# Performance work log

Hardware: AMD Instinct MI355X
Metric: run time of the kernel (lower is better)

Reference implementation:

```python
import jax, jax.numpy as jnp
import numpy as np

D = 256      # channels / model dim
HEADS = 8
DK = 32
DV = 32
B, H, W = 8, 32, 32
EPS = 1e-5


def setup_inputs() -> dict:
    key = jax.random.key(0)
    ks = jax.random.split(key, 9)
    s = 0.02
    return {
        "x":  jax.random.normal(ks[0], (B, D, H, W), dtype=jnp.float32),
        "Wq": jax.random.normal(ks[1], (HEADS * DK, D), dtype=jnp.float32) * s,
        "bq": jnp.zeros((HEADS * DK,), dtype=jnp.float32),
        "Wk": jax.random.normal(ks[2], (HEADS * DK, D), dtype=jnp.float32) * s,
        "bk": jnp.zeros((HEADS * DK,), dtype=jnp.float32),
        "Wv": jax.random.normal(ks[3], (HEADS * DV, D), dtype=jnp.float32) * s,
        "bv": jnp.zeros((HEADS * DV,), dtype=jnp.float32),
        "Wo": jax.random.normal(ks[4], (D, HEADS * DK), dtype=jnp.float32) * s,
        "bo": jnp.zeros((D,), dtype=jnp.float32),
    }


def reference(x, Wq, bq, Wk, bk, Wv, bv, Wo, bo):
    b, c, h, w = x.shape
    n = h * w
    # LayerNorm over [c, h, w] per sample, no affine (functional.layer_norm default)
    mu = jnp.mean(x, axis=(1, 2, 3), keepdims=True)
    var = jnp.var(x, axis=(1, 2, 3), keepdims=True)
    xn = (x - mu) * jax.lax.rsqrt(var + EPS)
    xr = xn.reshape(b, c, n).transpose(0, 2, 1)  # [b, n, c]

    def proj(Wt, bt, dh):
        y = xr @ Wt.T + bt                        # [b, n, heads*dh]
        return y.reshape(b, n, HEADS, dh).transpose(0, 2, 1, 3)  # [b, heads, n, dh]

    q = proj(Wq, bq, DK)
    k = proj(Wk, bk, DK)
    v = proj(Wv, bv, DV)

    scores = jnp.einsum('bhid,bhjd->bhij', q, k) * (DK ** -0.5)  # [b, heads, n, n]
    att = jax.nn.softmax(scores, axis=-1)
    tmp = jnp.einsum('bhij,bhjd->bhid', att, v)                  # [b, heads, n, dv]
    tmp = tmp.transpose(0, 2, 1, 3).reshape(b, n, HEADS * DV)    # [b, n, heads*dv]
    out = tmp @ Wo.T + bo                                        # [b, n, d]
    # NOTE: original does a raw .view(b, d, h, w) WITHOUT permuting — faithful reshape
    out = out.reshape(b, c, h, w)
    return out + x
```

## Files before the change

kernel.cpp:

```cpp
#include <hip/hip_runtime.h>
#include <stdint.h>

typedef unsigned short u16;
typedef unsigned int u32;
typedef __attribute__((ext_vector_type(8))) short bf16x8;
typedef __attribute__((ext_vector_type(4))) float f32x4;
typedef __attribute__((ext_vector_type(16))) float f32x16;

#define NTOK 1024
#define DMODEL 256
#define NHEAD 8
#define DK 32
#define NBATCH 8
#define PER_B (DMODEL * NTOK)

__device__ __forceinline__ float b2f(u16 h) {
    union { unsigned u; float f; } c; c.u = ((unsigned)h) << 16; return c.f;
}
__device__ __forceinline__ u16 f2b(float f) {
    unsigned u = __float_as_uint(f);
    unsigned r = u + 0x7fffu + ((u >> 16) & 1u);
    return (u16)(r >> 16);
}

__global__ void prep(const float* __restrict__ Wq, const float* __restrict__ Wk,
                     const float* __restrict__ Wv, const float* __restrict__ Wo,
                     u16* __restrict__ wb,
                     const float* __restrict__ x, float* __restrict__ part) {
    int bx = blockIdx.x;
    int t = threadIdx.x;
    if (bx < 256) {
        int m = bx >> 6;
        const float* W = (m == 0) ? Wq : (m == 1) ? Wk : (m == 2) ? Wv : Wo;
        int i = ((bx & 63) * 256 + t) * 4;
        float4 v = *(const float4*)&W[i];
        ushort4 o;
        o.x = f2b(v.x); o.y = f2b(v.y); o.z = f2b(v.z); o.w = f2b(v.w);
        *(ushort4*)&wb[m * 65536 + i] = o;
        return;
    }
    int blk = bx - 256;
    int b = blk >> 3, sl = blk & 7;
    int w = t >> 6, l = t & 63;
    const float* xb = x + (size_t)b * PER_B + sl * (PER_B / 8);
    float s = 0.f, ss = 0.f;
    for (int base = 0; base < PER_B / 8; base += 1024) {
        float4 v = *(const float4*)&xb[base + t * 4];
        s += v.x + v.y + v.z + v.w;
        ss += v.x * v.x + v.y * v.y + v.z * v.z + v.w * v.w;
    }
    for (int d = 1; d < 64; d <<= 1) {
        s += __shfl_xor(s, d, 64);
        ss += __shfl_xor(ss, d, 64);
    }
    __shared__ float red[2][4];
    if (l == 0) { red[0][w] = s; red[1][w] = ss; }
    __syncthreads();
    if (t == 0) {
        float S = red[0][0] + red[0][1] + red[0][2] + red[0][3];
        float SS = red[1][0] + red[1][1] + red[1][2] + red[1][3];
        part[(b * 8 + sl) * 2] = S;
        part[(b * 8 + sl) * 2 + 1] = SS;
    }
}

__global__ void normT(const float* __restrict__ x, const float* __restrict__ part,
                      u16* __restrict__ xn) {
    int b = blockIdx.z;
    int n0 = blockIdx.x * 32;
    int c0 = blockIdx.y * 32;
    int tx = threadIdx.x, ty = threadIdx.y;
    __shared__ float s_mu, s_rs;
    __shared__ float tile[32][33];
    if (tx == 0 && ty == 0) {
        float S = 0.f, SS = 0.f;
        for (int i = 0; i < 8; ++i) { S += part[(b * 8 + i) * 2]; SS += part[(b * 8 + i) * 2 + 1]; }
        float mu = S / (float)PER_B;
        float var = SS / (float)PER_B - mu * mu;
        s_mu = mu;
        s_rs = rsqrtf(var + 1e-5f);
    }
    __syncthreads();
    float mu = s_mu, rs = s_rs;
    const float* xb = x + (size_t)b * PER_B;
#pragma unroll
    for (int i = 0; i < 4; ++i) {
        int c = c0 + ty + i * 8;
        tile[ty + i * 8][tx] = (xb[c * NTOK + n0 + tx] - mu) * rs;
    }
    __syncthreads();
    u16* xnb = xn + (size_t)b * PER_B;
#pragma unroll
    for (int i = 0; i < 4; ++i) {
        int n = n0 + ty + i * 8;
        xnb[n * DMODEL + c0 + tx] = f2b(tile[tx][ty + i * 8]);
    }
}

__global__ __launch_bounds__(256, 4) void qkv_gemm(
    const u16* __restrict__ xn, const u16* __restrict__ wb,
    const float* __restrict__ bq, const float* __restrict__ bk,
    const float* __restrict__ bv,
    u16* __restrict__ qo, u16* __restrict__ ko, u16* __restrict__ vo) {
    int mt = blockIdx.x;
    int ot = blockIdx.y;
    int b = blockIdx.z;
    int sel = ot >> 2;
    int o0 = (ot & 3) * 64;
    const u16* W = wb + sel * 65536;
    const float* bias = (sel == 0) ? bq : (sel == 1) ? bk : bv;

    __shared__ u16 As[2][64][40];
    __shared__ u16 Bs[2][64][40];
    int t = threadIdx.x;
    int w = t >> 6, l = t & 63;
    int lr = t >> 2;
    int lc = (t & 3) * 8;
    int qd = l >> 4, ln = l & 15;

    const u16* xb = xn + ((size_t)b * NTOK + mt * 64) * DMODEL;

    {
        uint4 a0 = *(const uint4*)&xb[lr * DMODEL + lc];
        uint4 b0 = *(const uint4*)&W[(o0 + lr) * DMODEL + lc];
        *(uint4*)&As[0][lr][lc] = a0;
        *(uint4*)&Bs[0][lr][lc] = b0;
    }
    __syncthreads();

    f32x4 acc[4] = {};
#pragma unroll
    for (int kb = 0; kb < 8; ++kb) {
        int cur = kb & 1;
        uint4 a1, b1;
        if (kb < 7) {
            a1 = *(const uint4*)&xb[lr * DMODEL + (kb + 1) * 32 + lc];
            b1 = *(const uint4*)&W[(o0 + lr) * DMODEL + (kb + 1) * 32 + lc];
        }
        bf16x8 af = *(const bf16x8*)&As[cur][w * 16 + ln][qd * 8];
#pragma unroll
        for (int ns = 0; ns < 4; ++ns) {
            bf16x8 bf = *(const bf16x8*)&Bs[cur][ns * 16 + ln][qd * 8];
            acc[ns] = __builtin_amdgcn_mfma_f32_16x16x32_bf16(af, bf, acc[ns], 0, 0, 0);
        }
        if (kb < 7) {
            *(uint4*)&As[cur ^ 1][lr][lc] = a1;
            *(uint4*)&Bs[cur ^ 1][lr][lc] = b1;
            __syncthreads();
        }
    }
    if (sel == 0) {
        const float scale = 0.25505654344884634f;
#pragma unroll
        for (int ns = 0; ns < 4; ++ns) {
            int o = o0 + ns * 16 + ln;
            float bias_f = bias[o];
            int head = o >> 5, d = o & 31;
#pragma unroll
            for (int r = 0; r < 4; ++r) {
                int n_row = mt * 64 + w * 16 + qd * 4 + r;
                float v = (acc[ns][r] + bias_f) * scale;
                qo[(((size_t)b * NHEAD + head) * NTOK + n_row) * DK + d] = f2b(v);
            }
        }
    } else if (sel == 1) {
#pragma unroll
        for (int ns = 0; ns < 4; ++ns) {
            int o = o0 + ns * 16 + ln;
            float bias_f = bias[o];
            int head = o >> 5, d = o & 31;
            int dh = d >> 4, h8 = (d >> 3) & 1, j = d & 7;
            size_t base = (size_t)(b * NHEAD + head) * 32768;
#pragma unroll
            for (int r = 0; r < 4; ++r) {
                int n_row = mt * 64 + w * 16 + qd * 4 + r;
                int c = n_row >> 5, w5 = n_row & 31;
                int kslot = (w5 & 19) | ((w5 & 4) << 1) | ((w5 & 8) >> 1);
                float v = acc[ns][r] + bias_f;
                ko[base + ((size_t)((c * 2 + dh) * 2 + h8)) * 256 + kslot * 8 + j] = f2b(v);
            }
        }
    } else {
        int n0 = mt * 64 + w * 16 + qd * 4;
        int c = n0 >> 5, w5 = n0 & 31;
        int grp = (w5 >> 4) & 1, h8 = (w5 >> 3) & 1, j = w5 & 7;
#pragma unroll
        for (int ns = 0; ns < 4; ++ns) {
            int o = o0 + ns * 16 + ln;
            float bias_f = bias[o];
            int head = o >> 5, d = o & 31;
            ushort4 pk;
            pk.x = f2b(acc[ns][0] + bias_f);
            pk.y = f2b(acc[ns][1] + bias_f);
            pk.z = f2b(acc[ns][2] + bias_f);
            pk.w = f2b(acc[ns][3] + bias_f);
            size_t base = (size_t)(b * NHEAD + head) * 32768;
            *(ushort4*)&vo[base + ((size_t)((c * 2 + grp) * 2 + h8)) * 256 + d * 8 + j] = pk;
        }
    }
}

__global__ __launch_bounds__(256, 4) void attn(
    const u16* __restrict__ qws, const u16* __restrict__ kpan,
    const u16* __restrict__ vpan, u16* __restrict__ tmp) {
    int bh = blockIdx.x;
    int qp = blockIdx.y;
    int b = bh >> 3, h = bh & 7;
    const u16* Q  = qws + (size_t)bh * NTOK * DK;
    const u16* Kp = kpan + (size_t)bh * 32768;
    const u16* Vp = vpan + (size_t)bh * 32768;

    __shared__ float xl[2][64];
    __shared__ float xo[2][64][17];

    int t = threadIdx.x;
    int w = t >> 6, l = t & 63;
    int qsub = w >> 1, khalf = w & 1;
    int l31 = l & 31, hi = l >> 5;

    int q0 = qp * 64 + qsub * 32;
    int c0 = khalf * 16;

    bf16x8 qf0 = *(const bf16x8*)&Q[(q0 + l31) * DK + hi * 8];
    bf16x8 qf1 = *(const bf16x8*)&Q[(q0 + l31) * DK + 16 + hi * 8];

    const u16* kb = Kp + (size_t)c0 * 1024 + hi * 256 + l31 * 8;
    const u16* vb = Vp + (size_t)c0 * 1024 + hi * 256 + l31 * 8;

    f32x16 oacc = {};
    float lsum = 0.f;

#pragma unroll
    for (int c = 0; c < 16; ++c) {
        bf16x8 kf0 = *(const bf16x8*)&kb[c * 1024];
        bf16x8 kf1 = *(const bf16x8*)&kb[c * 1024 + 512];
        bf16x8 va  = *(const bf16x8*)&vb[c * 1024];
        bf16x8 vg  = *(const bf16x8*)&vb[c * 1024 + 512];

        f32x16 s = {};
        s = __builtin_amdgcn_mfma_f32_32x32x16_bf16(kf0, qf0, s, 0, 0, 0);
        s = __builtin_amdgcn_mfma_f32_32x32x16_bf16(kf1, qf1, s, 0, 0, 0);

        union { u32 u[4]; bf16x8 v; } pa, pb;
        float ps = 0.f;
#pragma unroll
        for (int j = 0; j < 4; ++j) {
            float e0 = __builtin_amdgcn_exp2f(s[2 * j]);
            float e1 = __builtin_amdgcn_exp2f(s[2 * j + 1]);
            float e2 = __builtin_amdgcn_exp2f(s[2 * j + 8]);
            float e3 = __builtin_amdgcn_exp2f(s[2 * j + 9]);
            ps += (e0 + e1) + (e2 + e3);
            pa.u[j] = __builtin_amdgcn_perm(__float_as_uint(e1), __float_as_uint(e0), 0x07060302u);
            pb.u[j] = __builtin_amdgcn_perm(__float_as_uint(e3), __float_as_uint(e2), 0x07060302u);
        }
        lsum += ps;

        oacc = __builtin_amdgcn_mfma_f32_32x32x16_bf16(va, pa.v, oacc, 0, 0, 0);
        oacc = __builtin_amdgcn_mfma_f32_32x32x16_bf16(vg, pb.v, oacc, 0, 0, 0);
    }

    if (khalf == 1) {
        xl[qsub][l] = lsum;
#pragma unroll
        for (int r = 0; r < 16; ++r) xo[qsub][l][r] = oacc[r];
    }
    __syncthreads();
    if (khalf == 0) {
        lsum += xl[qsub][l];
#pragma unroll
        for (int r = 0; r < 16; ++r) oacc[r] += xo[qsub][l][r];
        lsum += __shfl_xor(lsum, 32, 64);
        float linv = 1.0f / lsum;
        int qg = q0 + l31;
        u16* op = tmp + ((size_t)b * NTOK + qg) * DMODEL + h * DK;
#pragma unroll
        for (int g = 0; g < 4; ++g) {
            ushort4 pk;
            pk.x = f2b(oacc[g * 4 + 0] * linv);
            pk.y = f2b(oacc[g * 4 + 1] * linv);
            pk.z = f2b(oacc[g * 4 + 2] * linv);
            pk.w = f2b(oacc[g * 4 + 3] * linv);
            *(ushort4*)&op[g * 8 + hi * 4] = pk;
        }
    }
}

__global__ __launch_bounds__(256, 4) void oproj(
    const u16* __restrict__ tmp, const u16* __restrict__ wb,
    const float* __restrict__ bo, const float* __restrict__ x,
    float* __restrict__ out) {
    int mt = blockIdx.x;
    int ot = blockIdx.y;
    int b = blockIdx.z;
    const u16* Wo = wb + 3 * 65536;

    __shared__ u16 As[2][64][40];
    __shared__ u16 Bs[2][64][40];
    int t = threadIdx.x;
    int w = t >> 6, l = t & 63;
    int lr = t >> 2;
    int lc = (t & 3) * 8;
    int qd = l >> 4, ln = l & 15;

    const u16* ab = tmp + ((size_t)b * NTOK + mt * 64) * DMODEL;

    {
        uint4 a0 = *(const uint4*)&ab[lr * DMODEL + lc];
        uint4 b0 = *(const uint4*)&Wo[(ot * 64 + lr) * DMODEL + lc];
        *(uint4*)&As[0][lr][lc] = a0;
        *(uint4*)&Bs[0][lr][lc] = b0;
    }
    __syncthreads();

    f32x4 acc[4] = {};
#pragma unroll
    for (int kb = 0; kb < 8; ++kb) {
        int cur = kb & 1;
        uint4 a1, b1;
        if (kb < 7) {
            a1 = *(const uint4*)&ab[lr * DMODEL + (kb + 1) * 32 + lc];
            b1 = *(const uint4*)&Wo[(ot * 64 + lr) * DMODEL + (kb + 1) * 32 + lc];
        }
        bf16x8 af = *(const bf16x8*)&As[cur][w * 16 + ln][qd * 8];
#pragma unroll
        for (int ns = 0; ns < 4; ++ns) {
            bf16x8 bf = *(const bf16x8*)&Bs[cur][ns * 16 + ln][qd * 8];
            acc[ns] = __builtin_amdgcn_mfma_f32_16x16x32_bf16(af, bf, acc[ns], 0, 0, 0);
        }
        if (kb < 7) {
            *(uint4*)&As[cur ^ 1][lr][lc] = a1;
            *(uint4*)&Bs[cur ^ 1][lr][lc] = b1;
            __syncthreads();
        }
    }
    const float* xb = x + (size_t)b * PER_B;
    float* ob = out + (size_t)b * PER_B;
#pragma unroll
    for (int ns = 0; ns < 4; ++ns) {
        int o = ot * 64 + ns * 16 + ln;
        float bias_f = bo[o];
#pragma unroll
        for (int r = 0; r < 4; ++r) {
            int n_row = mt * 64 + w * 16 + qd * 4 + r;
            size_t idx = (size_t)n_row * DMODEL + o;
            ob[idx] = acc[ns][r] + bias_f + xb[idx];
        }
    }
}

extern "C" void kernel_launch(void* const* d_in, const int* in_sizes, int n_in,
                              void* d_out, int out_size, void* d_ws, size_t ws_size,
                              hipStream_t stream) {
    const float* x  = (const float*)d_in[0];
    const float* Wq = (const float*)d_in[1];
    const float* bq = (const float*)d_in[2];
    const float* Wk = (const float*)d_in[3];
    const float* bk = (const float*)d_in[4];
    const float* Wv = (const float*)d_in[5];
    const float* bv = (const float*)d_in[6];
    const float* Wo = (const float*)d_in[7];
    const float* bo = (const float*)d_in[8];
    float* out = (float*)d_out;

    char* ws = (char*)d_ws;
    float* part = (float*)ws;
    u16* wb  = (u16*)(ws + 1024);
    u16* xn  = (u16*)(ws + 1024 + (512u << 10));
    u16* qws = (u16*)(ws + 1024 + (512u << 10) + (4u << 20));
    u16* kws = (u16*)(ws + 1024 + (512u << 10) + (8u << 20));
    u16* vws = (u16*)(ws + 1024 + (512u << 10) + (12u << 20));
    u16* tmp = xn;

    hipLaunchKernelGGL(prep, dim3(320), dim3(256), 0, stream, Wq, Wk, Wv, Wo, wb, x, part);
    hipLaunchKernelGGL(normT, dim3(32, 8, 8), dim3(32, 8), 0, stream, x, part, xn);
    hipLaunchKernelGGL(qkv_gemm, dim3(16, 12, 8), dim3(256), 0, stream,
                       xn, wb, bq, bk, bv, qws, kws, vws);
    hipLaunchKernelGGL(attn, dim3(64, 16), dim3(256), 0, stream, qws, kws, vws, tmp);
    hipLaunchKernelGGL(oproj, dim3(16, 4, 8), dim3(256), 0, stream, tmp, wb, bo, x, out);
}
```

Before: 115.2 us.

## Fuse Q/K/V projections per block and interleave two key chunks in attention

```diff
diff --git a/kernel.cpp b/kernel.cpp
--- a/kernel.cpp
+++ b/kernel.cpp
@@ -103,15 +103,12 @@
     const float* __restrict__ bv,
     u16* __restrict__ qo, u16* __restrict__ ko, u16* __restrict__ vo) {
     int mt = blockIdx.x;
-    int ot = blockIdx.y;
+    int o64 = blockIdx.y;
     int b = blockIdx.z;
-    int sel = ot >> 2;
-    int o0 = (ot & 3) * 64;
-    const u16* W = wb + sel * 65536;
-    const float* bias = (sel == 0) ? bq : (sel == 1) ? bk : bv;
+    int o0 = o64 * 64;
 
     __shared__ u16 As[2][64][40];
-    __shared__ u16 Bs[2][64][40];
+    __shared__ u16 Bs[2][3][64][40];
     int t = threadIdx.x;
     int w = t >> 6, l = t & 63;
     int lr = t >> 2;
@@ -121,53 +118,63 @@
     const u16* xb = xn + ((size_t)b * NTOK + mt * 64) * DMODEL;
 
     {
-        uint4 a0 = *(const uint4*)&xb[lr * DMODEL + lc];
-        uint4 b0 = *(const uint4*)&W[(o0 + lr) * DMODEL + lc];
-        *(uint4*)&As[0][lr][lc] = a0;
-        *(uint4*)&Bs[0][lr][lc] = b0;
-    }
-    __syncthreads();
-
-    f32x4 acc[4] = {};
+        *(uint4*)&As[0][lr][lc] = *(const uint4*)&xb[lr * DMODEL + lc];
+#pragma unroll
+        for (int sel = 0; sel < 3; ++sel)
+            *(uint4*)&Bs[0][sel][lr][lc] =
+                *(const uint4*)&wb[sel * 65536 + (o0 + lr) * DMODEL + lc];
+    }
+    __syncthreads();
+
+    f32x4 acc[3][4] = {};
 #pragma unroll
     for (int kb = 0; kb < 8; ++kb) {
         int cur = kb & 1;
-        uint4 a1, b1;
+        uint4 a1, b1[3];
         if (kb < 7) {
             a1 = *(const uint4*)&xb[lr * DMODEL + (kb + 1) * 32 + lc];
-            b1 = *(const uint4*)&W[(o0 + lr) * DMODEL + (kb + 1) * 32 + lc];
+#pragma unroll
+            for (int sel = 0; sel < 3; ++sel)
+                b1[sel] = *(const uint4*)&wb[sel * 65536 + (o0 + lr) * DMODEL + (kb + 1) * 32 + lc];
         }
         bf16x8 af = *(const bf16x8*)&As[cur][w * 16 + ln][qd * 8];
 #pragma unroll
-        for (int ns = 0; ns < 4; ++ns) {
-            bf16x8 bf = *(const bf16x8*)&Bs[cur][ns * 16 + ln][qd * 8];
-            acc[ns] = __builtin_amdgcn_mfma_f32_16x16x32_bf16(af, bf, acc[ns], 0, 0, 0);
+        for (int sel = 0; sel < 3; ++sel) {
+#pragma unroll
+            for (int ns = 0; ns < 4; ++ns) {
+                bf16x8 bf = *(const bf16x8*)&Bs[cur][sel][ns * 16 + ln][qd * 8];
+                acc[sel][ns] = __builtin_amdgcn_mfma_f32_16x16x32_bf16(af, bf, acc[sel][ns], 0, 0, 0);
+            }
         }
         if (kb < 7) {
             *(uint4*)&As[cur ^ 1][lr][lc] = a1;
-            *(uint4*)&Bs[cur ^ 1][lr][lc] = b1;
+#pragma unroll
+            for (int sel = 0; sel < 3; ++sel)
+                *(uint4*)&Bs[cur ^ 1][sel][lr][lc] = b1[sel];
             __syncthreads();
         }
     }
-    if (sel == 0) {
+
+    {
         const float scale = 0.25505654344884634f;
 #pragma unroll
         for (int ns = 0; ns < 4; ++ns) {
             int o = o0 + ns * 16 + ln;
-            float bias_f = bias[o];
+            float bias_f = bq[o];
             int head = o >> 5, d = o & 31;
 #pragma unroll
             for (int r = 0; r < 4; ++r) {
                 int n_row = mt * 64 + w * 16 + qd * 4 + r;
-                float v = (acc[ns][r] + bias_f) * scale;
+                float v = (acc[0][ns][r] + bias_f) * scale;
                 qo[(((size_t)b * NHEAD + head) * NTOK + n_row) * DK + d] = f2b(v);
             }
         }
-    } else if (sel == 1) {
+    }
+    {
 #pragma unroll
         for (int ns = 0; ns < 4; ++ns) {
             int o = o0 + ns * 16 + ln;
-            float bias_f = bias[o];
+            float bias_f = bk[o];
             int head = o >> 5, d = o & 31;
             int dh = d >> 4, h8 = (d >> 3) & 1, j = d & 7;
             size_t base = (size_t)(b * NHEAD + head) * 32768;
@@ -176,31 +183,32 @@
                 int n_row = mt * 64 + w * 16 + qd * 4 + r;
                 int c = n_row >> 5, w5 = n_row & 31;
                 int kslot = (w5 & 19) | ((w5 & 4) << 1) | ((w5 & 8) >> 1);
-                float v = acc[ns][r] + bias_f;
+                float v = acc[1][ns][r] + bias_f;
                 ko[base + ((size_t)((c * 2 + dh) * 2 + h8)) * 256 + kslot * 8 + j] = f2b(v);
             }
         }
-    } else {
+    }
+    {
         int n0 = mt * 64 + w * 16 + qd * 4;
         int c = n0 >> 5, w5 = n0 & 31;
         int grp = (w5 >> 4) & 1, h8 = (w5 >> 3) & 1, j = w5 & 7;
 #pragma unroll
         for (int ns = 0; ns < 4; ++ns) {
             int o = o0 + ns * 16 + ln;
-            float bias_f = bias[o];
+            float bias_f = bv[o];
             int head = o >> 5, d = o & 31;
             ushort4 pk;
-            pk.x = f2b(acc[ns][0] + bias_f);
-            pk.y = f2b(acc[ns][1] + bias_f);
-            pk.z = f2b(acc[ns][2] + bias_f);
-            pk.w = f2b(acc[ns][3] + bias_f);
+            pk.x = f2b(acc[2][ns][0] + bias_f);
+            pk.y = f2b(acc[2][ns][1] + bias_f);
+            pk.z = f2b(acc[2][ns][2] + bias_f);
+            pk.w = f2b(acc[2][ns][3] + bias_f);
             size_t base = (size_t)(b * NHEAD + head) * 32768;
             *(ushort4*)&vo[base + ((size_t)((c * 2 + grp) * 2 + h8)) * 256 + d * 8 + j] = pk;
         }
     }
 }
 
-__global__ __launch_bounds__(256, 4) void attn(
+__global__ __launch_bounds__(256, 3) void attn(
     const u16* __restrict__ qws, const u16* __restrict__ kpan,
     const u16* __restrict__ vpan, u16* __restrict__ tmp) {
     int bh = blockIdx.x;
@@ -231,32 +239,48 @@
     float lsum = 0.f;
 
 #pragma unroll
-    for (int c = 0; c < 16; ++c) {
-        bf16x8 kf0 = *(const bf16x8*)&kb[c * 1024];
-        bf16x8 kf1 = *(const bf16x8*)&kb[c * 1024 + 512];
-        bf16x8 va  = *(const bf16x8*)&vb[c * 1024];
-        bf16x8 vg  = *(const bf16x8*)&vb[c * 1024 + 512];
-
-        f32x16 s = {};
-        s = __builtin_amdgcn_mfma_f32_32x32x16_bf16(kf0, qf0, s, 0, 0, 0);
-        s = __builtin_amdgcn_mfma_f32_32x32x16_bf16(kf1, qf1, s, 0, 0, 0);
-
-        union { u32 u[4]; bf16x8 v; } pa, pb;
-        float ps = 0.f;
+    for (int c = 0; c < 8; ++c) {
+        bf16x8 kf0a = *(const bf16x8*)&kb[c * 1024];
+        bf16x8 kf1a = *(const bf16x8*)&kb[c * 1024 + 512];
+        bf16x8 vaa  = *(const bf16x8*)&vb[c * 1024];
+        bf16x8 vga  = *(const bf16x8*)&vb[c * 1024 + 512];
+        bf16x8 kf0b = *(const bf16x8*)&kb[(c + 8) * 1024];
+        bf16x8 kf1b = *(const bf16x8*)&kb[(c + 8) * 1024 + 512];
+        bf16x8 vab  = *(const bf16x8*)&vb[(c + 8) * 1024];
+        bf16x8 vgb  = *(const bf16x8*)&vb[(c + 8) * 1024 + 512];
+
+        f32x16 sA = {};
+        sA = __builtin_amdgcn_mfma_f32_32x32x16_bf16(kf0a, qf0, sA, 0, 0, 0);
+        sA = __builtin_amdgcn_mfma_f32_32x32x16_bf16(kf1a, qf1, sA, 0, 0, 0);
+        f32x16 sB = {};
+        sB = __builtin_amdgcn_mfma_f32_32x32x16_bf16(kf0b, qf0, sB, 0, 0, 0);
+        sB = __builtin_amdgcn_mfma_f32_32x32x16_bf16(kf1b, qf1, sB, 0, 0, 0);
+
+        union { u32 u[4]; bf16x8 v; } paa, pba, pab, pbb;
+        float psA = 0.f, psB = 0.f;
 #pragma unroll
         for (int j = 0; j < 4; ++j) {
-            float e0 = __builtin_amdgcn_exp2f(s[2 * j]);
-            float e1 = __builtin_amdgcn_exp2f(s[2 * j + 1]);
-            float e2 = __builtin_amdgcn_exp2f(s[2 * j + 8]);
-            float e3 = __builtin_amdgcn_exp2f(s[2 * j + 9]);
-            ps += (e0 + e1) + (e2 + e3);
-            pa.u[j] = __builtin_amdgcn_perm(__float_as_uint(e1), __float_as_uint(e0), 0x07060302u);
-            pb.u[j] = __builtin_amdgcn_perm(__float_as_uint(e3), __float_as_uint(e2), 0x07060302u);
-        }
-        lsum += ps;
-
-        oacc = __builtin_amdgcn_mfma_f32_32x32x16_bf16(va, pa.v, oacc, 0, 0, 0);
-        oacc = __builtin_amdgcn_mfma_f32_32x32x16_bf16(vg, pb.v, oacc, 0, 0, 0);
+            float a0 = __builtin_amdgcn_exp2f(sA[2 * j]);
+            float a1 = __builtin_amdgcn_exp2f(sA[2 * j + 1]);
+            float a2 = __builtin_amdgcn_exp2f(sA[2 * j + 8]);
+            float a3 = __builtin_amdgcn_exp2f(sA[2 * j + 9]);
+            psA += (a0 + a1) + (a2 + a3);
+            paa.u[j] = __builtin_amdgcn_perm(__float_as_uint(a1), __float_as_uint(a0), 0x07060302u);
+            pba.u[j] = __builtin_amdgcn_perm(__float_as_uint(a3), __float_as_uint(a2), 0x07060302u);
+            float b0 = __builtin_amdgcn_exp2f(sB[2 * j]);
+            float b1 = __builtin_amdgcn_exp2f(sB[2 * j + 1]);
+            float b2 = __builtin_amdgcn_exp2f(sB[2 * j + 8]);
+            float b3 = __builtin_amdgcn_exp2f(sB[2 * j + 9]);
+            psB += (b0 + b1) + (b2 + b3);
+            pab.u[j] = __builtin_amdgcn_perm(__float_as_uint(b1), __float_as_uint(b0), 0x07060302u);
+            pbb.u[j] = __builtin_amdgcn_perm(__float_as_uint(b3), __float_as_uint(b2), 0x07060302u);
+        }
+        lsum += psA + psB;
+
+        oacc = __builtin_amdgcn_mfma_f32_32x32x16_bf16(vaa, paa.v, oacc, 0, 0, 0);
+        oacc = __builtin_amdgcn_mfma_f32_32x32x16_bf16(vga, pba.v, oacc, 0, 0, 0);
+        oacc = __builtin_amdgcn_mfma_f32_32x32x16_bf16(vab, pab.v, oacc, 0, 0, 0);
+        oacc = __builtin_amdgcn_mfma_f32_32x32x16_bf16(vgb, pbb.v, oacc, 0, 0, 0);
     }
 
     if (khalf == 1) {
@@ -373,7 +397,7 @@
 
     hipLaunchKernelGGL(prep, dim3(320), dim3(256), 0, stream, Wq, Wk, Wv, Wo, wb, x, part);
     hipLaunchKernelGGL(normT, dim3(32, 8, 8), dim3(32, 8), 0, stream, x, part, xn);
-    hipLaunchKernelGGL(qkv_gemm, dim3(16, 12, 8), dim3(256), 0, stream,
+    hipLaunchKernelGGL(qkv_gemm, dim3(16, 4, 8), dim3(256), 0, stream,
                        xn, wb, bq, bk, bv, qws, kws, vws);
     hipLaunchKernelGGL(attn, dim3(64, 16), dim3(256), 0, stream, qws, kws, vws, tmp);
     hipLaunchKernelGGL(oproj, dim3(16, 4, 8), dim3(256), 0, stream, tmp, wb, bo, x, out);
```

After: 119.5 us. +3.7%, slower.
